# Kernel optimization log

Hardware: AMD Instinct MI355X
Metric: run time of the kernel (lower is better)

## Reference

```python
import jax, jax.numpy as jnp
import numpy as np

B, C, T = 32, 128, 8192
NUM_CPNTS = 33


def setup_inputs() -> dict:
    key = jax.random.key(0)
    k1, k2, k3 = jax.random.split(key, 3)
    x = jax.random.normal(k1, (B, C, T), dtype=jnp.float32)
    # learned params: slopes [C, num_cpnts+1], biases [C]
    slopes = jax.random.normal(k2, (C, NUM_CPNTS + 1), dtype=jnp.float32) * 0.5 + 1.0
    biases = jax.random.normal(k3, (C,), dtype=jnp.float32) * 0.1
    return {"x": x, "slopes": slopes, "biases": biases}


def reference(x, slopes, biases):
    num_cpnts = slopes.shape[1] - 1
    delta_t = 2.0 / (num_cpnts - 1)
    cpnts = jnp.linspace(-1.0, 1.0, num_cpnts, dtype=x.dtype)  # [K]

    # bucket indices (constants w.r.t. grad, matching torch.no_grad block)
    ind1 = jnp.searchsorted(cpnts, x, side='right')   # [B,C,T] in [0, K]
    ind2 = jnp.maximum(ind1 - 1, 0)                   # [B,C,T] in [0, K-1]

    # cumulative biases per channel: [C, K]
    cum = jnp.cumsum(slopes[:, 1:-1] * delta_t, axis=1)           # [C, K-1]
    cumbias = jnp.concatenate([biases[:, None], cum + biases[:, None]], axis=1)

    cidx = jnp.arange(slopes.shape[0])[None, :, None]  # [1,C,1] channel index
    s = slopes[cidx, ind1]     # gather slope per element, [B,C,T]
    b = cumbias[cidx, ind2]    # gather cumulative bias, [B,C,T]
    cp = cpnts[ind2]           # left breakpoint, [B,C,T]
    return (x - cp) * s + b
```

## Files before the change

### kernel.cpp

```cpp
#include <hip/hip_runtime.h>

constexpr int kB = 32;
constexpr int kC = 128;
constexpr int kT = 8192;
constexpr int kK = 33;
constexpr float kDT = 2.0f / (kK - 1);
constexpr float kInvDT = (kK - 1) / 2.0f;

constexpr int kTab = kK + 2;

__device__ __forceinline__ float pwl_eval(float xv, const float2* __restrict__ tab) {
    float t = fmaf(xv, kInvDT, kInvDT);
    int fi = (int)floorf(t);
    int u = min(max(fi + 1, 0), kTab - 1);
    int i2 = min(max(fi, 0), kK - 1);
    float cp = fmaf((float)i2, kDT, -1.0f);
    float2 p = tab[u];
    return fmaf(xv - cp, p.x, p.y);
}

__global__ __launch_bounds__(256) void pwl_kernel(const float* __restrict__ x,
                                                  const float* __restrict__ slopes,
                                                  const float* __restrict__ biases,
                                                  float* __restrict__ out) {
    __shared__ float sl[kK + 1];
    __shared__ float2 tab[kTab];

    const int bc = blockIdx.x;
    const int c = bc & (kC - 1);
    const int tid = threadIdx.x;

    if (tid < kK + 1) sl[tid] = slopes[c * (kK + 1) + tid];
    __syncthreads();
    if (tid < kTab) {
        int su = min(tid, kK);
        int j = min(max(tid - 1, 0), kK - 1);
        float acc = biases[c];
        for (int i = 1; i <= j; ++i) acc = fmaf(sl[i], kDT, acc);
        tab[tid] = make_float2(sl[su], acc);
    }
    __syncthreads();

    const float4* __restrict__ xin = reinterpret_cast<const float4*>(x) + (size_t)bc * (kT / 4);
    float4* __restrict__ o = reinterpret_cast<float4*>(out) + (size_t)bc * (kT / 4);

    constexpr int kIters = (kT / 4) / 256;

    float4 v[kIters];
    #pragma unroll
    for (int k = 0; k < kIters; ++k) v[k] = xin[tid + k * 256];

    #pragma unroll
    for (int k = 0; k < kIters; ++k) {
        float4 r;
        r.x = pwl_eval(v[k].x, tab);
        r.y = pwl_eval(v[k].y, tab);
        r.z = pwl_eval(v[k].z, tab);
        r.w = pwl_eval(v[k].w, tab);
        o[tid + k * 256] = r;
    }
}

extern "C" void kernel_launch(void* const* d_in, const int* in_sizes, int n_in,
                              void* d_out, int out_size, void* d_ws, size_t ws_size,
                              hipStream_t stream) {
    const float* x = (const float*)d_in[0];
    const float* slopes = (const float*)d_in[1];
    const float* biases = (const float*)d_in[2];
    float* out = (float*)d_out;

    pwl_kernel<<<dim3(kB * kC), dim3(256), 0, stream>>>(x, slopes, biases, out);
}
```

Baseline: 233.0 us.

## Fold breakpoint offset into table bias, prefetch one ahead, nontemporal stores

```diff
diff --git a/kernel.cpp b/kernel.cpp
--- a/kernel.cpp
+++ b/kernel.cpp
@@ -7,16 +7,16 @@
 constexpr float kDT = 2.0f / (kK - 1);
 constexpr float kInvDT = (kK - 1) / 2.0f;
 
+typedef float floatx4 __attribute__((ext_vector_type(4)));
+
 constexpr int kTab = kK + 2;
 
 __device__ __forceinline__ float pwl_eval(float xv, const float2* __restrict__ tab) {
     float t = fmaf(xv, kInvDT, kInvDT);
     int fi = (int)floorf(t);
     int u = min(max(fi + 1, 0), kTab - 1);
-    int i2 = min(max(fi, 0), kK - 1);
-    float cp = fmaf((float)i2, kDT, -1.0f);
     float2 p = tab[u];
-    return fmaf(xv - cp, p.x, p.y);
+    return fmaf(xv, p.x, p.y);
 }
 
 __global__ __launch_bounds__(256) void pwl_kernel(const float* __restrict__ x,
@@ -34,30 +34,33 @@
     __syncthreads();
     if (tid < kTab) {
         int su = min(tid, kK);
-        int j = min(max(tid - 1, 0), kK - 1);
+        int i2 = min(max(tid - 1, 0), kK - 1);
         float acc = biases[c];
-        for (int i = 1; i <= j; ++i) acc = fmaf(sl[i], kDT, acc);
-        tab[tid] = make_float2(sl[su], acc);
+        for (int i = 1; i <= i2; ++i) acc = fmaf(sl[i], kDT, acc);
+        float s = sl[su];
+        float cp = fmaf((float)i2, kDT, -1.0f);
+        tab[tid] = make_float2(s, fmaf(-cp, s, acc));
     }
     __syncthreads();
 
-    const float4* __restrict__ xin = reinterpret_cast<const float4*>(x) + (size_t)bc * (kT / 4);
-    float4* __restrict__ o = reinterpret_cast<float4*>(out) + (size_t)bc * (kT / 4);
+    const floatx4* __restrict__ xin =
+        reinterpret_cast<const floatx4*>(x) + (size_t)bc * (kT / 4);
+    floatx4* __restrict__ o = reinterpret_cast<floatx4*>(out) + (size_t)bc * (kT / 4);
 
     constexpr int kIters = (kT / 4) / 256;
 
-    float4 v[kIters];
-    #pragma unroll
-    for (int k = 0; k < kIters; ++k) v[k] = xin[tid + k * 256];
-
+    floatx4 cur = xin[tid];
     #pragma unroll
     for (int k = 0; k < kIters; ++k) {
-        float4 r;
-        r.x = pwl_eval(v[k].x, tab);
-        r.y = pwl_eval(v[k].y, tab);
-        r.z = pwl_eval(v[k].z, tab);
-        r.w = pwl_eval(v[k].w, tab);
-        o[tid + k * 256] = r;
+        floatx4 nxt;
+        if (k + 1 < kIters) nxt = xin[tid + (k + 1) * 256];
+        floatx4 r;
+        r.x = pwl_eval(cur.x, tab);
+        r.y = pwl_eval(cur.y, tab);
+        r.z = pwl_eval(cur.z, tab);
+        r.w = pwl_eval(cur.w, tab);
+        __builtin_nontemporal_store(r, &o[tid + k * 256]);
+        cur = nxt;
     }
 }
 
```

After: 235.4 us. No clear change (+1.0%).
